# Performance work log

Measured on AMD Instinct MI355X. Metric: run time of the kernel, lower is better.

Reference implementation:

```python
import jax, jax.numpy as jnp
import numpy as np

B, Q, KV = 2, 2048, 2048
D_MODEL = 1024
N_HEADS = 16
D_KV = 64
EPS = 1e-6


def setup_inputs() -> dict:
    key = jax.random.key(0)
    ks = jax.random.split(key, 7)
    s = 0.02
    return {
        "hidden_states": jax.random.normal(ks[0], (B, Q, D_MODEL), jnp.float32),
        "key_value_states": jax.random.normal(ks[1], (B, KV, D_MODEL), jnp.float32),
        "wq": jax.random.normal(ks[2], (D_MODEL, N_HEADS * D_KV), jnp.float32) * s,
        "wk": jax.random.normal(ks[3], (D_MODEL, N_HEADS * D_KV), jnp.float32) * s,
        "wv": jax.random.normal(ks[4], (D_MODEL, N_HEADS * D_KV), jnp.float32) * s,
        "wo": jax.random.normal(ks[5], (N_HEADS * D_KV, D_MODEL), jnp.float32) * s,
        "norm_w": jnp.ones((D_MODEL,), jnp.float32),
    }


def reference(hidden_states, key_value_states, wq, wk, wv, wo, norm_w):
    # RMSNorm (T5-style, no mean subtraction)
    var = jnp.mean(jnp.square(hidden_states), axis=-1, keepdims=True)
    normed = hidden_states * jax.lax.rsqrt(var + EPS) * norm_w

    b, q_len, _ = hidden_states.shape
    kv_len = key_value_states.shape[1]

    def split_heads(x):  # [b, s, H*d] -> [b, H, s, d]
        return x.reshape(b, -1, N_HEADS, D_KV).transpose(0, 2, 1, 3)

    q = split_heads(normed @ wq)              # [b,H,q,d]
    k = split_heads(key_value_states @ wk)    # [b,H,kv,d]
    v = split_heads(key_value_states @ wv)    # [b,H,kv,d]

    # T5 attention: NO 1/sqrt(d) scaling; position_bias is zeros here
    # (has_relative_attention_bias=False, no mask) so it is a no-op.
    scores = jnp.einsum("bhqd,bhkd->bhqk", q, k)
    attn = jax.nn.softmax(scores.astype(jnp.float32), axis=-1).astype(scores.dtype)
    ctx = jnp.einsum("bhqk,bhkd->bhqd", attn, v)
    ctx = ctx.transpose(0, 2, 1, 3).reshape(b, q_len, N_HEADS * D_KV)
    attn_out = ctx @ wo

    # residual connection
    return hidden_states + attn_out
```

## Files before the change

### kernel.cpp

```cpp
#include <hip/hip_runtime.h>


typedef __attribute__((ext_vector_type(8))) short  s16x8;
typedef __attribute__((ext_vector_type(4))) float  f32x4;
typedef __attribute__((ext_vector_type(4))) int    i32x4;

#define LOG2E 1.4426950408889634f
#define EXP2(x) __builtin_amdgcn_exp2f(x)

__device__ __forceinline__ unsigned short f2bf(float f) {
  unsigned int u = __builtin_bit_cast(unsigned int, f);
  return (unsigned short)((u + 0x7FFFu + ((u >> 16) & 1u)) >> 16);
}

__device__ __forceinline__ unsigned cvtpk(float lo, float hi) {
  unsigned r;
  asm("v_cvt_pk_bf16_f32 %0, %1, %2" : "=v"(r) : "v"(lo), "v"(hi));
  return r;
}

__device__ __forceinline__ float f3max(float a, float b, float c) {
  return fmaxf(fmaxf(a, b), c);
}

__device__ __forceinline__ void gload16(const void* g, void* l) {
  __builtin_amdgcn_global_load_lds(
      (const __attribute__((address_space(1))) unsigned int*)g,
      (__attribute__((address_space(3))) unsigned int*)l, 16, 0, 0);
}

__global__ __launch_bounds__(256) void k_transpose4(
    const float* __restrict__ a0, const float* __restrict__ a1,
    const float* __restrict__ a2, const float* __restrict__ a3,
    unsigned short* __restrict__ o0, unsigned short* __restrict__ o1,
    unsigned short* __restrict__ o2, unsigned short* __restrict__ o3) {
  int z = blockIdx.z;
  const float* in = (z == 0) ? a0 : (z == 1) ? a1 : (z == 2) ? a2 : a3;
  unsigned short* out = (z == 0) ? o0 : (z == 1) ? o1 : (z == 2) ? o2 : o3;
  __shared__ float tile[64][65];
  int t = threadIdx.x;
  int tx = t & 15, ty = t >> 4;
  int r0 = blockIdx.y * 64, c0 = blockIdx.x * 64;
#pragma unroll
  for (int p = 0; p < 4; ++p) {
    int r = p * 16 + ty;
    float4 v = *reinterpret_cast<const float4*>(in + (size_t)(r0 + r) * 1024 + c0 + tx * 4);
    tile[r][tx * 4 + 0] = v.x; tile[r][tx * 4 + 1] = v.y;
    tile[r][tx * 4 + 2] = v.z; tile[r][tx * 4 + 3] = v.w;
  }
  __syncthreads();
#pragma unroll
  for (int p = 0; p < 4; ++p) {
    int c = p * 16 + ty;
    unsigned int lo = (unsigned int)f2bf(tile[tx * 4 + 0][c]) |
                      ((unsigned int)f2bf(tile[tx * 4 + 1][c]) << 16);
    unsigned int hi = (unsigned int)f2bf(tile[tx * 4 + 2][c]) |
                      ((unsigned int)f2bf(tile[tx * 4 + 3][c]) << 16);
    uint2 pk2; pk2.x = lo; pk2.y = hi;
    *reinterpret_cast<uint2*>(out + (size_t)(c0 + c) * 1024 + r0 + tx * 4) = pk2;
  }
}

__global__ __launch_bounds__(256) void k_prep(
    const float* __restrict__ hs, const float* __restrict__ w,
    unsigned short* __restrict__ normed,
    const float* __restrict__ kvs, unsigned short* __restrict__ kvb) {
  int t = threadIdx.x;
  if (blockIdx.x < 4096) {
    int row = blockIdx.x;
    float4 v = *reinterpret_cast<const float4*>(hs + (size_t)row * 1024 + t * 4);
    float s = v.x * v.x + v.y * v.y + v.z * v.z + v.w * v.w;
#pragma unroll
    for (int m = 1; m < 64; m <<= 1) s += __shfl_xor(s, m);
    __shared__ float ps[4];
    if ((t & 63) == 0) ps[t >> 6] = s;
    __syncthreads();
    float tot = ps[0] + ps[1] + ps[2] + ps[3];
    float sc = rsqrtf(tot * (1.0f / 1024.0f) + 1e-6f) * LOG2E;
    float4 wv = *reinterpret_cast<const float4*>(w + t * 4);
    unsigned int lo = (unsigned int)f2bf(v.x * sc * wv.x) |
                      ((unsigned int)f2bf(v.y * sc * wv.y) << 16);
    unsigned int hi = (unsigned int)f2bf(v.z * sc * wv.z) |
                      ((unsigned int)f2bf(v.w * sc * wv.w) << 16);
    uint2 pk2; pk2.x = lo; pk2.y = hi;
    *reinterpret_cast<uint2*>(normed + (size_t)row * 1024 + t * 4) = pk2;
  } else {
    int i = (blockIdx.x - 4096) * 256 + t;
    for (; i < 1048576; i += 1024 * 256) {
      float4 v = *reinterpret_cast<const float4*>(kvs + (size_t)i * 4);
      unsigned int lo = (unsigned int)f2bf(v.x) | ((unsigned int)f2bf(v.y) << 16);
      unsigned int hi = (unsigned int)f2bf(v.z) | ((unsigned int)f2bf(v.w) << 16);
      uint2 pk2; pk2.x = lo; pk2.y = hi;
      *reinterpret_cast<uint2*>(kvb + (size_t)i * 4) = pk2;
    }
  }
}

template <int BM>
__device__ __forceinline__ void gemm_body(
    const unsigned short* __restrict__ A, const unsigned short* __restrict__ Bt,
    void* __restrict__ Cout, const float* __restrict__ resid, int mode) {
  constexpr int MF = BM / 32;
  constexpr int ATILE = BM * 128;
  __shared__ __align__(16) char sm[2 * ATILE + 32768];
  int t = threadIdx.x;
  int bn = blockIdx.x, bm = blockIdx.y;
  int m0 = bm * BM, n0 = bn * 128;
  int lane = t & 63, w = t >> 6, lr = lane & 15, lg = lane >> 4;
  int wr = w >> 1, wc = w & 1;

  f32x4 acc[MF][4] = {};

  const char* aA = (const char*)A + ((size_t)(m0 + (t >> 3)) * 1024 + (t & 7) * 8) * 2;
  const char* aB = (const char*)Bt + ((size_t)(n0 + (t >> 3)) * 1024 + (t & 7) * 8) * 2;

  auto stage = [&](int buf, int kt) {
    int koff = kt * 128;
    char* As = sm + buf * ATILE;
    char* Bs = sm + 2 * ATILE + buf * 16384;
#pragma unroll
    for (int c = 0; c < BM / 32; ++c)
      gload16(aA + (size_t)c * 65536 + koff, As + c * 4096 + t * 16);
#pragma unroll
    for (int c = 0; c < 4; ++c)
      gload16(aB + (size_t)c * 65536 + koff, Bs + c * 4096 + t * 16);
  };

  stage(0, 0);
  __syncthreads();
  int cur = 0;
  for (int kt = 0; kt < 16; ++kt) {
    if (kt < 15) stage(cur ^ 1, kt + 1);
    const char* As = sm + cur * ATILE;
    const char* Bs = sm + 2 * ATILE + cur * 16384;
    s16x8 af[2][MF], bfr[2][4];
#pragma unroll
    for (int ks = 0; ks < 2; ++ks) {
#pragma unroll
      for (int m = 0; m < MF; ++m)
        af[ks][m] = *reinterpret_cast<const s16x8*>(
            As + (wr * (BM / 2) + m * 16 + lr) * 128 + ks * 64 + lg * 16);
#pragma unroll
      for (int n = 0; n < 4; ++n)
        bfr[ks][n] = *reinterpret_cast<const s16x8*>(
            Bs + (wc * 64 + n * 16 + lr) * 128 + ks * 64 + lg * 16);
    }
#pragma unroll
    for (int ks = 0; ks < 2; ++ks)
#pragma unroll
      for (int m = 0; m < MF; ++m)
#pragma unroll
        for (int n = 0; n < 4; ++n)
          acc[m][n] = __builtin_amdgcn_mfma_f32_16x16x32_bf16(af[ks][m], bfr[ks][n], acc[m][n], 0, 0, 0);
    __syncthreads();
    cur ^= 1;
  }

#pragma unroll
  for (int m = 0; m < MF; ++m)
#pragma unroll
    for (int n = 0; n < 4; ++n) {
      int colg = n0 + wc * 64 + n * 16 + lr;
      int rowb = m0 + wr * (BM / 2) + m * 16 + lg * 4;
      if (mode == 0) {
        unsigned short* C = (unsigned short*)Cout;
#pragma unroll
        for (int r = 0; r < 4; ++r)
          C[(size_t)(rowb + r) * 1024 + colg] = f2bf(acc[m][n][r]);
      } else if (mode == 1) {
        int h = colg >> 6, d = colg & 63;
        int b = rowb >> 11, kv = rowb & 2047;
        unsigned short* C = (unsigned short*)Cout +
            ((size_t)((b * 16 + h) * 64 + d) * 2048 + kv);
        unsigned int lo = (unsigned int)f2bf(acc[m][n][0]) |
                          ((unsigned int)f2bf(acc[m][n][1]) << 16);
        unsigned int hi = (unsigned int)f2bf(acc[m][n][2]) |
                          ((unsigned int)f2bf(acc[m][n][3]) << 16);
        uint2 pk2; pk2.x = lo; pk2.y = hi;
        *reinterpret_cast<uint2*>(C) = pk2;
      } else {
        float* C = (float*)Cout;
#pragma unroll
        for (int r = 0; r < 4; ++r) {
          size_t idx = (size_t)(rowb + r) * 1024 + colg;
          C[idx] = resid[idx] + acc[m][n][r];
        }
      }
    }
}

__global__ __launch_bounds__(256) void k_gemm_qkv(
    const unsigned short* __restrict__ normed, const unsigned short* __restrict__ kvb,
    const unsigned short* __restrict__ wqT, const unsigned short* __restrict__ wkT,
    const unsigned short* __restrict__ wvT,
    unsigned short* __restrict__ qb, unsigned short* __restrict__ kb,
    unsigned short* __restrict__ vTb) {
  int z = blockIdx.z;
  const unsigned short* A = (z == 0) ? normed : kvb;
  const unsigned short* B = (z == 0) ? wqT : (z == 1) ? wkT : wvT;
  void* C = (z == 0) ? (void*)qb : (z == 1) ? (void*)kb : (void*)vTb;
  gemm_body<128>(A, B, C, nullptr, (z == 2) ? 1 : 0);
}

__global__ __launch_bounds__(256) void k_gemm_o(
    const unsigned short* __restrict__ ctxb, const unsigned short* __restrict__ woT,
    float* __restrict__ out, const float* __restrict__ hs) {
  gemm_body<64>(ctxb, woT, (void*)out, hs, 2);
}

__global__ __launch_bounds__(512, 4) void k_attn(
    const unsigned short* __restrict__ q, const unsigned short* __restrict__ k,
    const unsigned short* __restrict__ vt, unsigned short* __restrict__ ctx) {
  __shared__ __align__(16) char sm[65536];
  int t = threadIdx.x, w = t >> 6, lane = t & 63, lr = lane & 15, lg = lane >> 4;

  int bid = blockIdx.x;
  int xcd = bid & 7, slot = bid >> 3;
  int bh = xcd * 4 + (slot >> 4);
  int qt = slot & 15;
  int b = bh >> 4, h = bh & 15;

  const char* qB = (const char*)q + ((size_t)(b * 2048 + qt * 128) * 1024 + h * 64) * 2;
  const char* kB = (const char*)k + ((size_t)(b * 2048) * 1024 + h * 64) * 2;
  const char* vB = (const char*)vt + (size_t)bh * 64 * 4096;

  int krow = t >> 3;
  int kcb  = ((t & 7) * 16) ^ ((krow & 7) << 4);
  int vrow = t >> 4;
  int vcb  = ((t & 15) * 16) ^ ((vrow & 7) << 4);

  auto stageKV = [&](int buf, int it2) {
    char* Kd = sm + buf * 16384;
    char* Vd = sm + 32768 + buf * 16384;
    const char* kb2 = kB + (size_t)(it2 * 128) * 2048;
    const char* vb2 = vB + it2 * 256;
#pragma unroll
    for (int c = 0; c < 2; ++c) {
      gload16(kb2 + (size_t)(c * 64 + krow) * 2048 + kcb, Kd + c * 8192 + t * 16);
      gload16(vb2 + (size_t)(c * 32 + vrow) * 4096 + vcb, Vd + c * 8192 + t * 16);
    }
  };

#pragma unroll
  for (int c = 0; c < 2; ++c)
    gload16(qB + (size_t)(c * 64 + krow) * 2048 + kcb, sm + c * 8192 + t * 16);
  __syncthreads();
  s16x8 qa[2];
#pragma unroll
  for (int ks = 0; ks < 2; ++ks) {
    int row = w * 16 + lr;
    qa[ks] = *reinterpret_cast<const s16x8*>(
        sm + row * 128 + ((ks * 64 + lg * 16) ^ ((lr & 7) << 4)));
  }
  __syncthreads();
  stageKV(0, 0);
  stageKV(1, 1);

  f32x4 octx[4] = {};
  float mrun = -1e30f;
  float lsum = 0.0f;

  for (int it = 0; it < 16; ++it) {
    if (it < 14) {
      asm volatile("s_waitcnt vmcnt(4)" ::: "memory");
    } else {
      asm volatile("s_waitcnt vmcnt(0)" ::: "memory");
    }
    __builtin_amdgcn_s_barrier();
    __builtin_amdgcn_sched_barrier(0);

    const char* Ks = sm + (it & 1) * 16384;
    const char* Vs = sm + 32768 + (it & 1) * 16384;

    f32x4 s2[8] = {};
    __builtin_amdgcn_s_setprio(1);
#pragma unroll
    for (int ks = 0; ks < 2; ++ks) {
      s16x8 ka[8];
#pragma unroll
      for (int n = 0; n < 8; ++n)
        ka[n] = *reinterpret_cast<const s16x8*>(
            Ks + (n * 16 + lr) * 128 + ((ks * 64 + lg * 16) ^ ((lr & 7) << 4)));
#pragma unroll
      for (int n = 0; n < 8; ++n)
        s2[n] = __builtin_amdgcn_mfma_f32_16x16x32_bf16(ka[n], qa[ks], s2[n], 0, 0, 0);
    }
    __builtin_amdgcn_s_setprio(0);

    float m2 = -1e30f;
#pragma unroll
    for (int n = 0; n < 8; ++n)
      m2 = f3max(f3max(m2, s2[n][0], s2[n][1]), s2[n][2], s2[n][3]);
    m2 = fmaxf(m2, __shfl_xor(m2, 16));
    m2 = fmaxf(m2, __shfl_xor(m2, 32));
    if (__any(m2 > mrun + 8.0f)) {
      float mx = fmaxf(mrun, m2);
      float sc = EXP2(mrun - mx);
      mrun = mx;
      lsum *= sc;
#pragma unroll
      for (int r = 0; r < 4; ++r) {
        float scr = __shfl(sc, lg * 4 + r);
#pragma unroll
        for (int nd = 0; nd < 4; ++nd) octx[nd][r] *= scr;
      }
    }

    unsigned pk[8][2];
    {
      float a0 = 0.0f, a1 = 0.0f, a2 = 0.0f, a3 = 0.0f;
#pragma unroll
      for (int n = 0; n < 8; ++n) {
        float p0 = EXP2(s2[n][0] - mrun);
        float p1 = EXP2(s2[n][1] - mrun);
        float p2 = EXP2(s2[n][2] - mrun);
        float p3 = EXP2(s2[n][3] - mrun);
        a0 += p0; a1 += p1; a2 += p2; a3 += p3;
        pk[n][0] = cvtpk(p0, p1);
        pk[n][1] = cvtpk(p2, p3);
      }
      lsum += (a0 + a1) + (a2 + a3);
    }

    __builtin_amdgcn_s_setprio(1);
#pragma unroll
    for (int ks = 0; ks < 4; ++ks) {
      s16x8 vb[4];
#pragma unroll
      for (int nd = 0; nd < 4; ++nd) {
        int row = nd * 16 + lr;
        int swz = (lr & 7) << 4;
        uint2 v1 = *reinterpret_cast<const uint2*>(
            Vs + row * 256 + ((ks * 64 + lg * 8) ^ swz));
        uint2 v2 = *reinterpret_cast<const uint2*>(
            Vs + row * 256 + ((ks * 64 + 32 + lg * 8) ^ swz));
        i32x4 vv; vv[0] = (int)v1.x; vv[1] = (int)v1.y;
        vv[2] = (int)v2.x; vv[3] = (int)v2.y;
        vb[nd] = __builtin_bit_cast(s16x8, vv);
      }
      i32x4 pv;
      pv[0] = (int)pk[2 * ks][0];     pv[1] = (int)pk[2 * ks][1];
      pv[2] = (int)pk[2 * ks + 1][0]; pv[3] = (int)pk[2 * ks + 1][1];
      s16x8 pa = __builtin_bit_cast(s16x8, pv);
#pragma unroll
      for (int nd = 0; nd < 4; ++nd)
        octx[nd] = __builtin_amdgcn_mfma_f32_16x16x32_bf16(pa, vb[nd], octx[nd], 0, 0, 0);
    }
    __builtin_amdgcn_s_setprio(0);

    __builtin_amdgcn_s_barrier();
    __builtin_amdgcn_sched_barrier(0);
    if (it < 14) stageKV(it & 1, it + 2);
  }

  {
    float tot = lsum;
    tot += __shfl_xor(tot, 16);
    tot += __shfl_xor(tot, 32);
    float inv = 1.0f / tot;
#pragma unroll
    for (int r = 0; r < 4; ++r) {
      float invr = __shfl(inv, lg * 4 + r);
      int qrow = qt * 128 + w * 16 + lg * 4 + r;
#pragma unroll
      for (int nd = 0; nd < 4; ++nd)
        ctx[(size_t)(b * 2048 + qrow) * 1024 + h * 64 + nd * 16 + lr] =
            f2bf(octx[nd][r] * invr);
    }
  }
}

extern "C" void kernel_launch(void* const* d_in, const int* in_sizes, int n_in,
                              void* d_out, int out_size, void* d_ws, size_t ws_size,
                              hipStream_t stream) {
  const float* hs  = (const float*)d_in[0];
  const float* kvs = (const float*)d_in[1];
  const float* wq  = (const float*)d_in[2];
  const float* wk  = (const float*)d_in[3];
  const float* wv  = (const float*)d_in[4];
  const float* wo  = (const float*)d_in[5];
  const float* nw  = (const float*)d_in[6];
  float* out = (float*)d_out;
  char* ws = (char*)d_ws;

  unsigned short* normed = (unsigned short*)(ws + (size_t)0);
  unsigned short* kvb    = (unsigned short*)(ws + ((size_t)8 << 20));
  unsigned short* wqT    = (unsigned short*)(ws + ((size_t)16 << 20));
  unsigned short* wkT    = (unsigned short*)(ws + ((size_t)18 << 20));
  unsigned short* wvT    = (unsigned short*)(ws + ((size_t)20 << 20));
  unsigned short* woT    = (unsigned short*)(ws + ((size_t)22 << 20));
  unsigned short* qb     = (unsigned short*)(ws + ((size_t)24 << 20));
  unsigned short* kb     = (unsigned short*)(ws + ((size_t)32 << 20));
  unsigned short* vTb    = (unsigned short*)(ws + ((size_t)40 << 20));
  unsigned short* ctxb   = (unsigned short*)(ws + ((size_t)48 << 20));

  k_transpose4<<<dim3(16, 16, 4), 256, 0, stream>>>(wq, wk, wv, wo, wqT, wkT, wvT, woT);
  k_prep<<<5120, 256, 0, stream>>>(hs, nw, normed, kvs, kvb);

  k_gemm_qkv<<<dim3(8, 32, 3), 256, 0, stream>>>(normed, kvb, wqT, wkT, wvT, qb, kb, vTb);

  k_attn<<<512, 512, 0, stream>>>(qb, kb, vTb, ctxb);

  k_gemm_o<<<dim3(8, 64), 256, 0, stream>>>(ctxb, woT, out, hs);
}
```

Baseline: 140.4 us.

## Use 32x32x16 MFMA in attention with 4 waves owning 32 query rows each

Rewrites the attention kernel's inner loop to use 32x32x16 bf16 MFMA instead of 16x16x32, with 256-thread blocks where each wave owns 32 query rows. The KV tile is processed in two halves of 64 keys to limit register pressure. Staging loops are adjusted to four loads per thread and the vmcnt wait is updated to match. The aim is fewer MFMA issues and fewer LDS reads per FLOP. In exchange each wave needs more registers and a block has fewer waves to hide latency.

Result: no change. 138.0 us (-1.7%).

```diff
diff --git a/kernel.cpp b/kernel.cpp
--- a/kernel.cpp
+++ b/kernel.cpp
@@ -1,9 +1,10 @@
 #include <hip/hip_runtime.h>
 
 
-typedef __attribute__((ext_vector_type(8))) short  s16x8;
-typedef __attribute__((ext_vector_type(4))) float  f32x4;
-typedef __attribute__((ext_vector_type(4))) int    i32x4;
+typedef __attribute__((ext_vector_type(8)))  short s16x8;
+typedef __attribute__((ext_vector_type(4)))  float f32x4;
+typedef __attribute__((ext_vector_type(16))) float f32x16;
+typedef __attribute__((ext_vector_type(4)))  int   i32x4;
 
 #define LOG2E 1.4426950408889634f
 #define EXP2(x) __builtin_amdgcn_exp2f(x)
@@ -208,11 +209,12 @@
   gemm_body<64>(ctxb, woT, (void*)out, hs, 2);
 }
 
-__global__ __launch_bounds__(512, 4) void k_attn(
+__global__ __launch_bounds__(256, 2) void k_attn(
     const unsigned short* __restrict__ q, const unsigned short* __restrict__ k,
     const unsigned short* __restrict__ vt, unsigned short* __restrict__ ctx) {
   __shared__ __align__(16) char sm[65536];
-  int t = threadIdx.x, w = t >> 6, lane = t & 63, lr = lane & 15, lg = lane >> 4;
+  int t = threadIdx.x, w = t >> 6, lane = t & 63;
+  int l5 = lane & 31, hi = lane >> 5, l7 = lane & 7;
 
   int bid = blockIdx.x;
   int xcd = bid & 7, slot = bid >> 3;
@@ -235,34 +237,34 @@
     const char* kb2 = kB + (size_t)(it2 * 128) * 2048;
     const char* vb2 = vB + it2 * 256;
 #pragma unroll
-    for (int c = 0; c < 2; ++c) {
-      gload16(kb2 + (size_t)(c * 64 + krow) * 2048 + kcb, Kd + c * 8192 + t * 16);
-      gload16(vb2 + (size_t)(c * 32 + vrow) * 4096 + vcb, Vd + c * 8192 + t * 16);
+    for (int c = 0; c < 4; ++c) {
+      gload16(kb2 + (size_t)(c * 32 + krow) * 2048 + kcb, Kd + c * 4096 + t * 16);
+      gload16(vb2 + (size_t)(c * 16 + vrow) * 4096 + vcb, Vd + c * 4096 + t * 16);
     }
   };
 
 #pragma unroll
-  for (int c = 0; c < 2; ++c)
-    gload16(qB + (size_t)(c * 64 + krow) * 2048 + kcb, sm + c * 8192 + t * 16);
+  for (int c = 0; c < 4; ++c)
+    gload16(qB + (size_t)(c * 32 + krow) * 2048 + kcb, sm + c * 4096 + t * 16);
   __syncthreads();
-  s16x8 qa[2];
-#pragma unroll
-  for (int ks = 0; ks < 2; ++ks) {
-    int row = w * 16 + lr;
-    qa[ks] = *reinterpret_cast<const s16x8*>(
-        sm + row * 128 + ((ks * 64 + lg * 16) ^ ((lr & 7) << 4)));
+  s16x8 qa[4];
+#pragma unroll
+  for (int s = 0; s < 4; ++s) {
+    int row = w * 32 + l5;
+    qa[s] = *reinterpret_cast<const s16x8*>(
+        sm + row * 128 + ((32 * s + 16 * hi) ^ (l7 << 4)));
   }
   __syncthreads();
   stageKV(0, 0);
   stageKV(1, 1);
 
-  f32x4 octx[4] = {};
+  f32x16 octx[2] = {};
   float mrun = -1e30f;
   float lsum = 0.0f;
 
   for (int it = 0; it < 16; ++it) {
     if (it < 14) {
-      asm volatile("s_waitcnt vmcnt(4)" ::: "memory");
+      asm volatile("s_waitcnt vmcnt(8)" ::: "memory");
     } else {
       asm volatile("s_waitcnt vmcnt(0)" ::: "memory");
     }
@@ -272,81 +274,82 @@
     const char* Ks = sm + (it & 1) * 16384;
     const char* Vs = sm + 32768 + (it & 1) * 16384;
 
-    f32x4 s2[8] = {};
-    __builtin_amdgcn_s_setprio(1);
-#pragma unroll
-    for (int ks = 0; ks < 2; ++ks) {
-      s16x8 ka[8];
-#pragma unroll
-      for (int n = 0; n < 8; ++n)
-        ka[n] = *reinterpret_cast<const s16x8*>(
-            Ks + (n * 16 + lr) * 128 + ((ks * 64 + lg * 16) ^ ((lr & 7) << 4)));
-#pragma unroll
-      for (int n = 0; n < 8; ++n)
-        s2[n] = __builtin_amdgcn_mfma_f32_16x16x32_bf16(ka[n], qa[ks], s2[n], 0, 0, 0);
-    }
-    __builtin_amdgcn_s_setprio(0);
-
-    float m2 = -1e30f;
-#pragma unroll
-    for (int n = 0; n < 8; ++n)
-      m2 = f3max(f3max(m2, s2[n][0], s2[n][1]), s2[n][2], s2[n][3]);
-    m2 = fmaxf(m2, __shfl_xor(m2, 16));
-    m2 = fmaxf(m2, __shfl_xor(m2, 32));
-    if (__any(m2 > mrun + 8.0f)) {
-      float mx = fmaxf(mrun, m2);
-      float sc = EXP2(mrun - mx);
-      mrun = mx;
-      lsum *= sc;
-#pragma unroll
-      for (int r = 0; r < 4; ++r) {
-        float scr = __shfl(sc, lg * 4 + r);
-#pragma unroll
-        for (int nd = 0; nd < 4; ++nd) octx[nd][r] *= scr;
+#pragma unroll
+    for (int hh = 0; hh < 2; ++hh) {
+      f32x16 s2[2] = {};
+      __builtin_amdgcn_s_setprio(1);
+#pragma unroll
+      for (int kb = 0; kb < 2; ++kb) {
+        int kvb = hh * 2 + kb;
+#pragma unroll
+        for (int s = 0; s < 4; ++s) {
+          s16x8 ka = *reinterpret_cast<const s16x8*>(
+              Ks + (kvb * 32 + l5) * 128 + ((32 * s + 16 * hi) ^ (l7 << 4)));
+          s2[kb] = __builtin_amdgcn_mfma_f32_32x32x16_bf16(ka, qa[s], s2[kb], 0, 0, 0);
+        }
       }
-    }
-
-    unsigned pk[8][2];
-    {
-      float a0 = 0.0f, a1 = 0.0f, a2 = 0.0f, a3 = 0.0f;
-#pragma unroll
-      for (int n = 0; n < 8; ++n) {
-        float p0 = EXP2(s2[n][0] - mrun);
-        float p1 = EXP2(s2[n][1] - mrun);
-        float p2 = EXP2(s2[n][2] - mrun);
-        float p3 = EXP2(s2[n][3] - mrun);
-        a0 += p0; a1 += p1; a2 += p2; a3 += p3;
-        pk[n][0] = cvtpk(p0, p1);
-        pk[n][1] = cvtpk(p2, p3);
+      __builtin_amdgcn_s_setprio(0);
+
+      float m2 = -1e30f;
+#pragma unroll
+      for (int kb = 0; kb < 2; ++kb)
+#pragma unroll
+        for (int r = 0; r < 16; r += 2)
+          m2 = f3max(m2, s2[kb][r], s2[kb][r + 1]);
+      m2 = fmaxf(m2, __shfl_xor(m2, 32));
+      if (__any(m2 > mrun + 8.0f)) {
+        float mx = fmaxf(mrun, m2);
+        float sc = EXP2(mrun - mx);
+        mrun = mx;
+        lsum *= sc;
+#pragma unroll
+        for (int r = 0; r < 16; ++r) {
+          float scr = __shfl(sc, (r & 3) + 8 * (r >> 2) + 4 * hi);
+          octx[0][r] *= scr;
+          octx[1][r] *= scr;
+        }
       }
-      lsum += (a0 + a1) + (a2 + a3);
-    }
-
-    __builtin_amdgcn_s_setprio(1);
-#pragma unroll
-    for (int ks = 0; ks < 4; ++ks) {
-      s16x8 vb[4];
-#pragma unroll
-      for (int nd = 0; nd < 4; ++nd) {
-        int row = nd * 16 + lr;
-        int swz = (lr & 7) << 4;
-        uint2 v1 = *reinterpret_cast<const uint2*>(
-            Vs + row * 256 + ((ks * 64 + lg * 8) ^ swz));
-        uint2 v2 = *reinterpret_cast<const uint2*>(
-            Vs + row * 256 + ((ks * 64 + 32 + lg * 8) ^ swz));
-        i32x4 vv; vv[0] = (int)v1.x; vv[1] = (int)v1.y;
-        vv[2] = (int)v2.x; vv[3] = (int)v2.y;
-        vb[nd] = __builtin_bit_cast(s16x8, vv);
+
+#pragma unroll
+      for (int kb = 0; kb < 2; ++kb) {
+        int kvb = hh * 2 + kb;
+        float p[16];
+        float a0 = 0.0f, a1 = 0.0f;
+#pragma unroll
+        for (int r = 0; r < 16; r += 2) {
+          p[r]     = EXP2(s2[kb][r] - mrun);
+          p[r + 1] = EXP2(s2[kb][r + 1] - mrun);
+          a0 += p[r]; a1 += p[r + 1];
+        }
+        lsum += a0 + a1;
+        i32x4 pf[2];
+#pragma unroll
+        for (int s = 0; s < 2; ++s) {
+          pf[s][0] = (int)cvtpk(p[8 * s + 0], p[8 * s + 1]);
+          pf[s][1] = (int)cvtpk(p[8 * s + 2], p[8 * s + 3]);
+          pf[s][2] = (int)cvtpk(p[8 * s + 4], p[8 * s + 5]);
+          pf[s][3] = (int)cvtpk(p[8 * s + 6], p[8 * s + 7]);
+        }
+        __builtin_amdgcn_s_setprio(1);
+#pragma unroll
+        for (int dt = 0; dt < 2; ++dt) {
+          int row = dt * 32 + l5;
+          const char* vbase = Vs + row * 256;
+#pragma unroll
+          for (int s = 0; s < 2; ++s) {
+            int coff = 64 * kvb + 32 * s + 8 * hi;
+            uint2 v1 = *reinterpret_cast<const uint2*>(vbase + (coff ^ (l7 << 4)));
+            uint2 v2 = *reinterpret_cast<const uint2*>(vbase + ((coff + 16) ^ (l7 << 4)));
+            i32x4 vv; vv[0] = (int)v1.x; vv[1] = (int)v1.y;
+            vv[2] = (int)v2.x; vv[3] = (int)v2.y;
+            octx[dt] = __builtin_amdgcn_mfma_f32_32x32x16_bf16(
+                __builtin_bit_cast(s16x8, pf[s]),
+                __builtin_bit_cast(s16x8, vv), octx[dt], 0, 0, 0);
+          }
+        }
+        __builtin_amdgcn_s_setprio(0);
       }
-      i32x4 pv;
-      pv[0] = (int)pk[2 * ks][0];     pv[1] = (int)pk[2 * ks][1];
-      pv[2] = (int)pk[2 * ks + 1][0]; pv[3] = (int)pk[2 * ks + 1][1];
-      s16x8 pa = __builtin_bit_cast(s16x8, pv);
-#pragma unroll
-      for (int nd = 0; nd < 4; ++nd)
-        octx[nd] = __builtin_amdgcn_mfma_f32_16x16x32_bf16(pa, vb[nd], octx[nd], 0, 0, 0);
-    }
-    __builtin_amdgcn_s_setprio(0);
+    }
 
     __builtin_amdgcn_s_barrier();
     __builtin_amdgcn_sched_barrier(0);
@@ -354,18 +357,17 @@
   }
 
   {
-    float tot = lsum;
-    tot += __shfl_xor(tot, 16);
-    tot += __shfl_xor(tot, 32);
+    float tot = lsum + __shfl_xor(lsum, 32);
     float inv = 1.0f / tot;
 #pragma unroll
-    for (int r = 0; r < 4; ++r) {
-      float invr = __shfl(inv, lg * 4 + r);
-      int qrow = qt * 128 + w * 16 + lg * 4 + r;
-#pragma unroll
-      for (int nd = 0; nd < 4; ++nd)
-        ctx[(size_t)(b * 2048 + qrow) * 1024 + h * 64 + nd * 16 + lr] =
-            f2bf(octx[nd][r] * invr);
+    for (int r = 0; r < 16; ++r) {
+      int qrow = (r & 3) + 8 * (r >> 2) + 4 * hi;
+      float invr = __shfl(inv, qrow);
+      int grow = qt * 128 + w * 32 + qrow;
+#pragma unroll
+      for (int dt = 0; dt < 2; ++dt)
+        ctx[(size_t)(b * 2048 + grow) * 1024 + h * 64 + dt * 32 + l5] =
+            f2bf(octx[dt][r] * invr);
     }
   }
 }
@@ -399,7 +401,7 @@
 
   k_gemm_qkv<<<dim3(8, 32, 3), 256, 0, stream>>>(normed, kvb, wqT, wkT, wvT, qb, kb, vTb);
 
-  k_attn<<<512, 512, 0, stream>>>(qb, kb, vTb, ctxb);
+  k_attn<<<512, 256, 0, stream>>>(qb, kb, vTb, ctxb);
 
   k_gemm_o<<<dim3(8, 64), 256, 0, stream>>>(ctxb, woT, out, hs);
 }
```
